# Kernel optimization log

Hardware: AMD Instinct MI355X
Metric: run time of the kernel (lower is better)

## Reference

```python
import jax, jax.numpy as jnp
import numpy as np

B, S, E, H, NQ = 8, 2048, 8, 2, 8
D = E // H  # head_dim = 4
DIM = 2 ** NQ  # 256-amplitude state vector

# CNOT chain pattern from the module: (0,1),(1,2),...,(NQ-2,NQ-1),(NQ-1,0)
CNOTS = [(i, i + 1) for i in range(NQ - 1)] + [(NQ - 1, 0)]

# Pauli-Z sign table: wire 0 is the most-significant qubit axis (torchquantum convention)
_k = np.arange(DIM)
_SIGNS = (1.0 - 2.0 * ((_k[None, :] >> (NQ - 1 - np.arange(NQ))[:, None]) & 1)).astype(np.float32)  # (NQ, DIM)


def _quantum_measure(tok):
    """Batched simulation of the per-token circuit. tok: (N, E) real -> (N, NQ) <Z> values."""
    n = tok.shape[0]
    idx = jnp.arange(NQ) % D
    # encoder RX(tok[w]) then explicit RX(tok[w % head_dim]) on each wire: angles add.
    half = 0.5 * (tok[:, :NQ] + tok[:, idx])  # (N, NQ)
    a0 = jnp.cos(half).astype(jnp.complex64)
    a1 = (-1j) * jnp.sin(half).astype(jnp.complex64)
    qub = jnp.stack([a0, a1], axis=-1)  # (N, NQ, 2) per-qubit states (product state before CNOTs)
    # Kronecker product across the fixed NQ wires
    state = qub[:, 0, :]
    for w in range(1, NQ):
        state = (state[:, :, None] * qub[:, w, None, :]).reshape(n, -1)
    state = state.reshape((n,) + (2,) * NQ)
    # CNOT chain: flip target axis within control=1 block
    for c, t in CNOTS:
        c0 = jax.lax.index_in_dim(state, 0, c + 1, keepdims=True)
        c1 = jnp.flip(jax.lax.index_in_dim(state, 1, c + 1, keepdims=True), axis=t + 1)
        state = jnp.concatenate([c0, c1], axis=c + 1)
    p = (state.real ** 2 + state.imag ** 2).reshape(n, DIM)  # probabilities
    return p @ jnp.asarray(_SIGNS.T)  # (N, NQ) Pauli-Z expectations


def setup_inputs() -> dict:
    key = jax.random.key(0)
    ks = jax.random.split(key, 5)
    sc = 1.0 / np.sqrt(E)
    return {
        "x": jax.random.normal(ks[0], (B, S, E), jnp.float32),
        "Wq": jax.random.normal(ks[1], (E, E), jnp.float32) * sc,
        "Wk": jax.random.normal(ks[2], (E, E), jnp.float32) * sc,
        "Wv": jax.random.normal(ks[3], (E, E), jnp.float32) * sc,
        "Wo": jax.random.normal(ks[4], (E, E), jnp.float32) * sc,
    }


def reference(x, Wq, Wk, Wv, Wo):
    b, s, _ = x.shape
    # nn.Linear(bias=False): y = x @ W^T
    q = jnp.einsum('bse,fe->bsf', x, Wq).reshape(b, s, H, D)
    k = jnp.einsum('bse,fe->bsf', x, Wk).reshape(b, s, H, D)
    v = jnp.einsum('bse,fe->bsf', x, Wv).reshape(b, s, H, D)
    scores = jnp.einsum('bihd,bjhd->bhij', q, k) / jnp.sqrt(jnp.float32(D))
    attn = jax.nn.softmax(scores, axis=-1)  # dropout is identity at inference
    out = jnp.einsum('bhij,bjhd->bihd', attn, v).reshape(b, s, E)
    z = _quantum_measure(out.reshape(-1, E)).reshape(b, s, NQ)  # NQ == E
    return jnp.einsum('bsq,fq->bsf', z, Wo)
```

## Files before the change

### kernel.cpp

```cpp
#include <hip/hip_runtime.h>


#define SS 2048
#define EE 8

__device__ __forceinline__ float rl(float v, int t) {
    return __int_as_float(__builtin_amdgcn_readlane(__float_as_int(v), t));
}

extern "C" __global__ __launch_bounds__(256)
void qa_attn2(const float* __restrict__ x, const float* __restrict__ Wq,
              const float* __restrict__ Wk, const float* __restrict__ Wv,
              float* __restrict__ wsD, float4* __restrict__ wsA) {
    __shared__ float wrow[96];
    const int bid = blockIdx.x;
    const int jq = bid & 3, rt = (bid >> 2) & 7, h = (bid >> 5) & 1, b = bid >> 6;
    const int tid = threadIdx.x, lane = tid & 63, w = tid >> 6;

    if (tid < 96) {
        const int grp = tid >> 5, d = (tid >> 3) & 3, e = tid & 7;
        const float* W = (grp == 0) ? Wq : (grp == 1 ? Wk : Wv);
        float val = W[(h * 4 + d) * EE + e];
        if (grp == 0) val *= 0.72134752044f;
        wrow[tid] = val;
    }
    __syncthreads();

    float q[4][4];
    const int row0 = rt * 256 + lane;
    #pragma unroll
    for (int m = 0; m < 4; ++m) {
        const float* xp = x + ((size_t)(b * SS + row0 + m * 64)) * EE;
        float xv[8];
        *(float4*)&xv[0] = *(const float4*)xp;
        *(float4*)&xv[4] = *(const float4*)(xp + 4);
        #pragma unroll
        for (int d = 0; d < 4; ++d) {
            float s = 0.f;
            #pragma unroll
            for (int e = 0; e < 8; ++e) s += xv[e] * wrow[d * 8 + e];
            q[m][d] = s;
        }
    }

    float den[4] = {0.f, 0.f, 0.f, 0.f};
    float acc[4][4] = {};

    const int jbase = jq * 512 + w * 128;
    #pragma unroll 1
    for (int g = 0; g < 2; ++g) {
        const int myj = jbase + g * 64 + lane;
        const float* xp = x + ((size_t)(b * SS + myj)) * EE;
        float xv[8];
        *(float4*)&xv[0] = *(const float4*)xp;
        *(float4*)&xv[4] = *(const float4*)(xp + 4);
        float mk[4], mv[4];
        #pragma unroll
        for (int d = 0; d < 4; ++d) {
            float sk = 0.f, sv = 0.f;
            #pragma unroll
            for (int e = 0; e < 8; ++e) {
                sk += xv[e] * wrow[32 + d * 8 + e];
                sv += xv[e] * wrow[64 + d * 8 + e];
            }
            mk[d] = sk; mv[d] = sv;
        }
        #pragma unroll 16
        for (int t = 0; t < 64; ++t) {
            const float k0 = rl(mk[0], t), k1 = rl(mk[1], t),
                        k2 = rl(mk[2], t), k3 = rl(mk[3], t);
            const float v0 = rl(mv[0], t), v1 = rl(mv[1], t),
                        v2 = rl(mv[2], t), v3 = rl(mv[3], t);
            #pragma unroll
            for (int m = 0; m < 4; ++m) {
                const float s = q[m][0] * k0 + q[m][1] * k1 + q[m][2] * k2 + q[m][3] * k3;
                const float e = __builtin_amdgcn_exp2f(s);
                den[m] += e;
                acc[m][0] += e * v0; acc[m][1] += e * v1;
                acc[m][2] += e * v2; acc[m][3] += e * v3;
            }
        }
    }

    const int slice = jq * 4 + w;
    #pragma unroll
    for (int m = 0; m < 4; ++m) {
        const size_t idx = ((size_t)((b * 2 + h) * 16 + slice)) * SS + row0 + m * 64;
        wsD[idx] = den[m];
        wsA[idx] = make_float4(acc[m][0], acc[m][1], acc[m][2], acc[m][3]);
    }
}

extern "C" __global__ __launch_bounds__(256)
void qa_quantum2(const float* __restrict__ wsD, const float4* __restrict__ wsA,
                 const float* __restrict__ Wo, float* __restrict__ out) {
    __shared__ float wo[64];
    const int tid = threadIdx.x;
    if (tid < 64) wo[tid] = Wo[tid];
    __syncthreads();

    const int g = blockIdx.x * 256 + tid;
    const int b = g >> 11, s = g & 2047;

    float tok[8];
    #pragma unroll
    for (int h = 0; h < 2; ++h) {
        float den = 0.f, a0 = 0.f, a1 = 0.f, a2 = 0.f, a3 = 0.f;
        #pragma unroll
        for (int sl = 0; sl < 16; ++sl) {
            const size_t idx = ((size_t)((b * 2 + h) * 16 + sl)) * SS + s;
            den += wsD[idx];
            const float4 p = wsA[idx];
            a0 += p.x; a1 += p.y; a2 += p.z; a3 += p.w;
        }
        const float inv = 1.f / den;
        tok[h * 4 + 0] = a0 * inv; tok[h * 4 + 1] = a1 * inv;
        tok[h * 4 + 2] = a2 * inv; tok[h * 4 + 3] = a3 * inv;
    }

    float c[8];
    #pragma unroll
    for (int ww = 0; ww < 8; ++ww) c[ww] = __cosf(tok[ww] + tok[ww & 3]);

    float z[8];
    float p = 1.f;
    #pragma unroll
    for (int qq = 1; qq < 8; ++qq) { p *= c[qq]; z[qq] = p; }
    z[0] = p;
    #pragma unroll
    for (int qq = 1; qq < 8; ++qq) z[qq] *= c[0];

    float y[8];
    #pragma unroll
    for (int f = 0; f < 8; ++f) {
        float sum = 0.f;
        #pragma unroll
        for (int qq = 0; qq < 8; ++qq) sum += z[qq] * wo[f * 8 + qq];
        y[f] = sum;
    }
    float* op = out + (size_t)g * 8;
    *(float4*)op       = make_float4(y[0], y[1], y[2], y[3]);
    *(float4*)(op + 4) = make_float4(y[4], y[5], y[6], y[7]);
}

extern "C" void kernel_launch(void* const* d_in, const int* in_sizes, int n_in,
                              void* d_out, int out_size, void* d_ws, size_t ws_size,
                              hipStream_t stream) {
    const float* x  = (const float*)d_in[0];
    const float* Wq = (const float*)d_in[1];
    const float* Wk = (const float*)d_in[2];
    const float* Wv = (const float*)d_in[3];
    const float* Wo = (const float*)d_in[4];
    float* out = (float*)d_out;

    float*  wsD = (float*)d_ws;
    float4* wsA = (float4*)((char*)d_ws + (8 * 2 * 16 * 2048) * sizeof(float));

    qa_attn2<<<dim3(512), dim3(256), 0, stream>>>(x, Wq, Wk, Wv, wsD, wsA);
    qa_quantum2<<<dim3(64), dim3(256), 0, stream>>>(wsD, wsA, Wo, out);
}
```

Baseline: 96.04 us.

## Stage K/V in LDS, widen query tile to 8 rows, reduce wave partials in-block

Measured after the change: 87.24 us. -9.2%, faster.

```diff
diff --git a/kernel.cpp b/kernel.cpp
--- a/kernel.cpp
+++ b/kernel.cpp
@@ -4,17 +4,17 @@
 #define SS 2048
 #define EE 8
 
-__device__ __forceinline__ float rl(float v, int t) {
-    return __int_as_float(__builtin_amdgcn_readlane(__float_as_int(v), t));
-}
-
 extern "C" __global__ __launch_bounds__(256)
-void qa_attn2(const float* __restrict__ x, const float* __restrict__ Wq,
+void qa_attn3(const float* __restrict__ x, const float* __restrict__ Wq,
               const float* __restrict__ Wk, const float* __restrict__ Wv,
               float* __restrict__ wsD, float4* __restrict__ wsA) {
     __shared__ float wrow[96];
+    __shared__ __align__(16) float4 kv4[512];
+    __shared__ __align__(16) float4 racc[4 * 512];
+    __shared__ float rden[4 * 512];
+
     const int bid = blockIdx.x;
-    const int jq = bid & 3, rt = (bid >> 2) & 7, h = (bid >> 5) & 1, b = bid >> 6;
+    const int jw = bid & 7, rt = (bid >> 3) & 3, h = (bid >> 5) & 1, b = bid >> 6;
     const int tid = threadIdx.x, lane = tid & 63, w = tid >> 6;
 
     if (tid < 96) {
@@ -26,10 +26,31 @@
     }
     __syncthreads();
 
-    float q[4][4];
-    const int row0 = rt * 256 + lane;
+    {
+        const int j = jw * 256 + tid;
+        const float* xp = x + ((size_t)(b * SS + j)) * EE;
+        float xv[8];
+        *(float4*)&xv[0] = *(const float4*)xp;
+        *(float4*)&xv[4] = *(const float4*)(xp + 4);
+        float kk[4], vv[4];
+        #pragma unroll
+        for (int d = 0; d < 4; ++d) {
+            float sk = 0.f, sv = 0.f;
+            #pragma unroll
+            for (int e = 0; e < 8; ++e) {
+                sk += xv[e] * wrow[32 + d * 8 + e];
+                sv += xv[e] * wrow[64 + d * 8 + e];
+            }
+            kk[d] = sk; vv[d] = sv;
+        }
+        kv4[tid * 2]     = make_float4(kk[0], kk[1], kk[2], kk[3]);
+        kv4[tid * 2 + 1] = make_float4(vv[0], vv[1], vv[2], vv[3]);
+    }
+
+    float q[8][4];
+    const int row0 = rt * 512 + lane;
     #pragma unroll
-    for (int m = 0; m < 4; ++m) {
+    for (int m = 0; m < 8; ++m) {
         const float* xp = x + ((size_t)(b * SS + row0 + m * 64)) * EE;
         float xv[8];
         *(float4*)&xv[0] = *(const float4*)xp;
@@ -42,57 +63,50 @@
             q[m][d] = s;
         }
     }
+    __syncthreads();
 
-    float den[4] = {0.f, 0.f, 0.f, 0.f};
-    float acc[4][4] = {};
-
-    const int jbase = jq * 512 + w * 128;
-    #pragma unroll 1
-    for (int g = 0; g < 2; ++g) {
-        const int myj = jbase + g * 64 + lane;
-        const float* xp = x + ((size_t)(b * SS + myj)) * EE;
-        float xv[8];
-        *(float4*)&xv[0] = *(const float4*)xp;
-        *(float4*)&xv[4] = *(const float4*)(xp + 4);
-        float mk[4], mv[4];
+    float den[8] = {};
+    float acc[8][4] = {};
+    const int jb = w * 64;
+    #pragma unroll 2
+    for (int jl = 0; jl < 64; ++jl) {
+        const float4 kk = kv4[(jb + jl) * 2];
+        const float4 vv = kv4[(jb + jl) * 2 + 1];
         #pragma unroll
-        for (int d = 0; d < 4; ++d) {
-            float sk = 0.f, sv = 0.f;
-            #pragma unroll
-            for (int e = 0; e < 8; ++e) {
-                sk += xv[e] * wrow[32 + d * 8 + e];
-                sv += xv[e] * wrow[64 + d * 8 + e];
-            }
-            mk[d] = sk; mv[d] = sv;
-        }
-        #pragma unroll 16
-        for (int t = 0; t < 64; ++t) {
-            const float k0 = rl(mk[0], t), k1 = rl(mk[1], t),
-                        k2 = rl(mk[2], t), k3 = rl(mk[3], t);
-            const float v0 = rl(mv[0], t), v1 = rl(mv[1], t),
-                        v2 = rl(mv[2], t), v3 = rl(mv[3], t);
-            #pragma unroll
-            for (int m = 0; m < 4; ++m) {
-                const float s = q[m][0] * k0 + q[m][1] * k1 + q[m][2] * k2 + q[m][3] * k3;
-                const float e = __builtin_amdgcn_exp2f(s);
-                den[m] += e;
-                acc[m][0] += e * v0; acc[m][1] += e * v1;
-                acc[m][2] += e * v2; acc[m][3] += e * v3;
-            }
+        for (int m = 0; m < 8; ++m) {
+            const float s = q[m][0] * kk.x + q[m][1] * kk.y
+                          + q[m][2] * kk.z + q[m][3] * kk.w;
+            const float e = __builtin_amdgcn_exp2f(s);
+            den[m] += e;
+            acc[m][0] += e * vv.x; acc[m][1] += e * vv.y;
+            acc[m][2] += e * vv.z; acc[m][3] += e * vv.w;
         }
     }
 
-    const int slice = jq * 4 + w;
     #pragma unroll
-    for (int m = 0; m < 4; ++m) {
-        const size_t idx = ((size_t)((b * 2 + h) * 16 + slice)) * SS + row0 + m * 64;
-        wsD[idx] = den[m];
-        wsA[idx] = make_float4(acc[m][0], acc[m][1], acc[m][2], acc[m][3]);
+    for (int m = 0; m < 8; ++m) {
+        rden[w * 512 + lane + m * 64] = den[m];
+        racc[w * 512 + lane + m * 64] =
+            make_float4(acc[m][0], acc[m][1], acc[m][2], acc[m][3]);
+    }
+    __syncthreads();
+    #pragma unroll
+    for (int u = 0; u < 2; ++u) {
+        const int r = tid + u * 256;
+        float d = rden[r] + rden[512 + r] + rden[1024 + r] + rden[1536 + r];
+        float4 a0 = racc[r], a1 = racc[512 + r], a2 = racc[1024 + r], a3 = racc[1536 + r];
+        float4 a = make_float4(a0.x + a1.x + a2.x + a3.x,
+                               a0.y + a1.y + a2.y + a3.y,
+                               a0.z + a1.z + a2.z + a3.z,
+                               a0.w + a1.w + a2.w + a3.w);
+        const size_t idx = ((size_t)((b * 2 + h) * 8 + jw)) * SS + rt * 512 + r;
+        wsD[idx] = d;
+        wsA[idx] = a;
     }
 }
 
 extern "C" __global__ __launch_bounds__(256)
-void qa_quantum2(const float* __restrict__ wsD, const float4* __restrict__ wsA,
+void qa_quantum3(const float* __restrict__ wsD, const float4* __restrict__ wsA,
                  const float* __restrict__ Wo, float* __restrict__ out) {
     __shared__ float wo[64];
     const int tid = threadIdx.x;
@@ -107,8 +121,8 @@
     for (int h = 0; h < 2; ++h) {
         float den = 0.f, a0 = 0.f, a1 = 0.f, a2 = 0.f, a3 = 0.f;
         #pragma unroll
-        for (int sl = 0; sl < 16; ++sl) {
-            const size_t idx = ((size_t)((b * 2 + h) * 16 + sl)) * SS + s;
+        for (int sl = 0; sl < 8; ++sl) {
+            const size_t idx = ((size_t)((b * 2 + h) * 8 + sl)) * SS + s;
             den += wsD[idx];
             const float4 p = wsA[idx];
             a0 += p.x; a1 += p.y; a2 += p.z; a3 += p.w;
@@ -154,8 +168,8 @@
     float* out = (float*)d_out;
 
     float*  wsD = (float*)d_ws;
-    float4* wsA = (float4*)((char*)d_ws + (8 * 2 * 16 * 2048) * sizeof(float));
+    float4* wsA = (float4*)((char*)d_ws + (16 * 8 * 2048) * sizeof(float));
 
-    qa_attn2<<<dim3(512), dim3(256), 0, stream>>>(x, Wq, Wk, Wv, wsD, wsA);
-    qa_quantum2<<<dim3(64), dim3(256), 0, stream>>>(wsD, wsA, Wo, out);
+    qa_attn3<<<dim3(512), dim3(256), 0, stream>>>(x, Wq, Wk, Wv, wsD, wsA);
+    qa_quantum3<<<dim3(64), dim3(256), 0, stream>>>(wsD, wsA, Wo, out);
 }
```
